# Optimization experiments

Measured on AMD Instinct MI355X. Metric: run time of the kernel, lower is better.

Reference implementation:

```python
import jax, jax.numpy as jnp
import numpy as np

LN_EPS = 1e-5

def _layernorm(x, scale, bias):
    mu = jnp.mean(x, axis=-1, keepdims=True)
    var = jnp.var(x, axis=-1, keepdims=True)
    return (x - mu) * jax.lax.rsqrt(var + LN_EPS) * scale + bias

def setup_inputs() -> dict:
    T, node_num, num_nodes, E, C = 4, 10000, 50000, 256, 128
    key = jax.random.key(0)
    ks = jax.random.split(key, 12)
    s = lambda fan_in: 1.0 / np.sqrt(fan_in)
    return {
        "x": jax.random.normal(ks[0], (T * node_num, E), jnp.float32),
        "batched_x": jax.random.normal(ks[1], (num_nodes, E), jnp.float32),
        "indices": jax.random.randint(ks[2], (T, node_num), 0, num_nodes, jnp.int32),
        "ln_d_scale": jnp.ones((E,), jnp.float32),
        "ln_d_bias": jnp.zeros((E,), jnp.float32),
        "W1_d": jax.random.normal(ks[3], (E, 2 * E), jnp.float32) * s(E),
        "b1_d": jnp.zeros((2 * E,), jnp.float32),
        "W2_d": jax.random.normal(ks[4], (2 * E, C), jnp.float32) * s(2 * E),
        "b2_d": jnp.zeros((C,), jnp.float32),
        "ln_u_scale": jnp.ones((C,), jnp.float32),
        "ln_u_bias": jnp.zeros((C,), jnp.float32),
        "W1_u": jax.random.normal(ks[5], (C, 2 * C), jnp.float32) * s(C),
        "b1_u": jnp.zeros((2 * C,), jnp.float32),
        "W2_u": jax.random.normal(ks[6], (2 * C, E), jnp.float32) * s(2 * C),
        "b2_u": jnp.zeros((E,), jnp.float32),
    }

def reference(x, batched_x, indices, ln_d_scale, ln_d_bias, W1_d, b1_d, W2_d, b2_d,
              ln_u_scale, ln_u_bias, W1_u, b1_u, W2_u, b2_u):
    T, node_num = indices.shape
    num_nodes, E = batched_x.shape
    xr = x.reshape(T, node_num, E)
    # _to_entire: per-step scatter-add of active-node embeddings into the full node table
    def scatter_one(xi, idx):
        return jnp.zeros((num_nodes, E), x.dtype).at[idx].add(xi)
    ta = jax.vmap(scatter_one)(xr, indices)          # [T, num_nodes, E]
    inp = ta + batched_x[None]                        # broadcast entire features
    h = _layernorm(inp, ln_d_scale, ln_d_bias)
    h = jax.nn.gelu(h @ W1_d + b1_d, approximate=False) @ W2_d + b2_d  # [T, num_nodes, C]
    # _from_entire: gather each step's active nodes back, concat, LN + MLP up
    g = jnp.take_along_axis(h, indices[..., None], axis=1)  # [T, node_num, C]
    g = g.reshape(T * node_num, -1)
    g = _layernorm(g, ln_u_scale, ln_u_bias)
    out = jax.nn.gelu(g @ W1_u + b1_u, approximate=False) @ W2_u + b2_u  # [T*node_num, E]
    return out
```

## Files before the change

kernel.cpp:

```cpp
#include <hip/hip_runtime.h>
#include <math.h>

#define T_STEPS   4
#define NODE_NUM  10000
#define NUM_NODES 50000
#define E         256
#define TWO_E     512
#define CC        128
#define TWO_C     256
#define ROWS      32

typedef short bf16x8 __attribute__((ext_vector_type(8)));
typedef float f32x4  __attribute__((ext_vector_type(4)));

#define MFMA16(a, b, c) __builtin_amdgcn_mfma_f32_16x16x32_bf16((a), (b), (c), 0, 0, 0)

static __device__ unsigned short g_wt[294912];

__device__ __forceinline__ float geluf(float v) {
    return 0.5f * v * (1.0f + erff(v * 0.70710678118654752440f));
}

__device__ __forceinline__ unsigned short f2bf(float f) {
    unsigned int u = __builtin_bit_cast(unsigned int, f);
    u += 0x7fffu + ((u >> 16) & 1u);
    return (unsigned short)(u >> 16);
}

__global__ void prep_weights(const float* __restrict__ W1d, const float* __restrict__ W2d,
                             const float* __restrict__ W1u, const float* __restrict__ W2u) {
    int i = blockIdx.x * 256 + threadIdx.x;
    if (i < 131072) {
        int n = i >> 8, k = i & 255;
        g_wt[i] = f2bf(W1d[(size_t)k * TWO_E + n]);
    }
    if (i < 65536) {
        int n = i >> 9, k = i & 511;
        g_wt[131072 + i] = f2bf(W2d[(size_t)k * CC + n]);
    }
    if (i < 32768) {
        int n = i >> 7, k = i & 127;
        g_wt[196608 + i] = f2bf(W1u[(size_t)k * TWO_C + n]);
    }
    if (i < 65536) {
        int n = i >> 8, k = i & 255;
        g_wt[229376 + i] = f2bf(W2u[(size_t)k * E + n]);
    }
}

__global__ void zero_rows_kernel(float* __restrict__ table,
                                 const int* __restrict__ indices,
                                 int gr0, int t0) {
    int gr = gr0 + blockIdx.x * 4 + (threadIdx.x >> 6);
    int trel = gr / NODE_NUM - t0;
    int idx = indices[gr];
    int c = (threadIdx.x & 63) * 4;
    float4 z = make_float4(0.f, 0.f, 0.f, 0.f);
    *reinterpret_cast<float4*>(&table[((size_t)trel * NUM_NODES + idx) * E + c]) = z;
}

__global__ void scatter_kernel(float* __restrict__ table,
                               const float* __restrict__ x,
                               const int* __restrict__ indices,
                               int gr0, int t0) {
    int gr = gr0 + blockIdx.x;
    int trel = gr / NODE_NUM - t0;
    int idx = indices[gr];
    atomicAdd(&table[((size_t)trel * NUM_NODES + idx) * E + threadIdx.x],
              x[(size_t)gr * E + threadIdx.x]);
}

__global__ __launch_bounds__(256, 3)
void mlp_kernel(const float* __restrict__ table,
                const float* __restrict__ batched_x,
                const int* __restrict__ indices,
                const float* __restrict__ lnd_s, const float* __restrict__ lnd_b,
                const float* __restrict__ b1d, const float* __restrict__ b2d,
                const float* __restrict__ lnu_s, const float* __restrict__ lnu_b,
                const float* __restrict__ b1u, const float* __restrict__ b2u,
                float* __restrict__ out,
                int gr0, int t0, int grLim) {
    __shared__ __align__(16) unsigned char smem[50176];
    __shared__ size_t rbase[ROWS];
    __shared__ int    ridx[ROWS];

    float*          Xf  = (float*)smem;
    unsigned short* Xs  = (unsigned short*)(smem + 33280);
    unsigned short* H1  = (unsigned short*)smem;
    float*          H2f = (float*)(smem + 33280);
    unsigned short* H2b = (unsigned short*)smem;
    unsigned short* G1  = (unsigned short*)(smem + 8704);

    const unsigned short* w1t  = g_wt;
    const unsigned short* w2t  = g_wt + 131072;
    const unsigned short* w1ut = g_wt + 196608;
    const unsigned short* w2ut = g_wt + 229376;

    const int tid = threadIdx.x;
    const int w = tid >> 6, lane = tid & 63;
    const int l16 = lane & 15, quad = lane >> 4;
    const int grb = gr0 + blockIdx.x * ROWS;

    if (tid < ROWS) {
        int gr = grb + tid;
        if (gr >= grLim) gr = grLim - 1;
        int trel = gr / NODE_NUM - t0;
        int idx = indices[gr];
        rbase[tid] = ((size_t)trel * NUM_NODES + idx) * E;
        ridx[tid]  = idx;
    }
    __syncthreads();

    #pragma unroll
    for (int it = 0; it < 8; ++it) {
        int v = it * 256 + tid;
        int r = v >> 6;
        int c = (v & 63) * 4;
        float4 tv = *reinterpret_cast<const float4*>(&table[rbase[r] + c]);
        float4 bv = *reinterpret_cast<const float4*>(&batched_x[(size_t)ridx[r] * E + c]);
        float4 s; s.x = tv.x + bv.x; s.y = tv.y + bv.y; s.z = tv.z + bv.z; s.w = tv.w + bv.w;
        *reinterpret_cast<float4*>(&Xf[r * 260 + c]) = s;
    }
    __syncthreads();

    {
        int row = tid >> 3, l8 = tid & 7;
        float s = 0.f, sq = 0.f;
        #pragma unroll
        for (int k = 0; k < 32; ++k) {
            float v = Xf[row * 260 + k * 8 + l8];
            s += v; sq += v * v;
        }
        s  += __shfl_xor(s, 1);  s  += __shfl_xor(s, 2);  s  += __shfl_xor(s, 4);
        sq += __shfl_xor(sq, 1); sq += __shfl_xor(sq, 2); sq += __shfl_xor(sq, 4);
        float mu = s * (1.0f / E);
        float var = sq * (1.0f / E) - mu * mu;
        float rs = rsqrtf(var + 1e-5f);
        #pragma unroll
        for (int k = 0; k < 32; ++k) {
            int c = k * 8 + l8;
            float v = (Xf[row * 260 + c] - mu) * rs * lnd_s[c] + lnd_b[c];
            Xs[row * 264 + c] = f2bf(v);
        }
    }
    __syncthreads();

    {
        bf16x8 af[2][8];
        #pragma unroll
        for (int mt = 0; mt < 2; ++mt) {
            const unsigned short* base = Xs + (l16 + 16 * mt) * 264 + quad * 8;
            #pragma unroll
            for (int ks = 0; ks < 8; ++ks)
                af[mt][ks] = *reinterpret_cast<const bf16x8*>(base + ks * 32);
        }
        #pragma unroll
        for (int nt_ = 0; nt_ < 8; ++nt_) {
            int n = (w * 8 + nt_) * 16 + l16;
            const unsigned short* bp = w1t + (size_t)n * 256 + quad * 8;
            f32x4 a0 = {0.f, 0.f, 0.f, 0.f}, a1 = {0.f, 0.f, 0.f, 0.f};
            #pragma unroll
            for (int ks = 0; ks < 8; ++ks) {
                bf16x8 b = *reinterpret_cast<const bf16x8*>(bp + ks * 32);
                a0 = MFMA16(af[0][ks], b, a0);
                a1 = MFMA16(af[1][ks], b, a1);
            }
            float bias = b1d[n];
            #pragma unroll
            for (int reg = 0; reg < 4; ++reg) {
                int r = quad * 4 + reg;
                H1[r * 520 + n]        = f2bf(geluf(a0[reg] + bias));
                H1[(r + 16) * 520 + n] = f2bf(geluf(a1[reg] + bias));
            }
        }
    }
    __syncthreads();

    {
        f32x4 acc2[2][2];
        #pragma unroll
        for (int i = 0; i < 2; ++i)
            #pragma unroll
            for (int j = 0; j < 2; ++j) acc2[i][j] = (f32x4){0.f, 0.f, 0.f, 0.f};
        #pragma unroll
        for (int kh = 0; kh < 2; ++kh) {
            bf16x8 af2[2][8];
            #pragma unroll
            for (int mt = 0; mt < 2; ++mt) {
                const unsigned short* base = H1 + (l16 + 16 * mt) * 520 + kh * 256 + quad * 8;
                #pragma unroll
                for (int ks = 0; ks < 8; ++ks)
                    af2[mt][ks] = *reinterpret_cast<const bf16x8*>(base + ks * 32);
            }
            #pragma unroll
            for (int nt2 = 0; nt2 < 2; ++nt2) {
                int n = (w * 2 + nt2) * 16 + l16;
                const unsigned short* bp = w2t + (size_t)n * 512 + kh * 256 + quad * 8;
                #pragma unroll
                for (int ks = 0; ks < 8; ++ks) {
                    bf16x8 b = *reinterpret_cast<const bf16x8*>(bp + ks * 32);
                    acc2[nt2][0] = MFMA16(af2[0][ks], b, acc2[nt2][0]);
                    acc2[nt2][1] = MFMA16(af2[1][ks], b, acc2[nt2][1]);
                }
            }
        }
        #pragma unroll
        for (int nt2 = 0; nt2 < 2; ++nt2) {
            int n = (w * 2 + nt2) * 16 + l16;
            float bias = b2d[n];
            #pragma unroll
            for (int mt = 0; mt < 2; ++mt)
                #pragma unroll
                for (int reg = 0; reg < 4; ++reg) {
                    int r = mt * 16 + quad * 4 + reg;
                    H2f[r * 132 + n] = acc2[nt2][mt][reg] + bias;
                }
        }
    }
    __syncthreads();

    {
        int row = tid >> 3, l8 = tid & 7;
        float s = 0.f, sq = 0.f;
        #pragma unroll
        for (int k = 0; k < 16; ++k) {
            float v = H2f[row * 132 + k * 8 + l8];
            s += v; sq += v * v;
        }
        s  += __shfl_xor(s, 1);  s  += __shfl_xor(s, 2);  s  += __shfl_xor(s, 4);
        sq += __shfl_xor(sq, 1); sq += __shfl_xor(sq, 2); sq += __shfl_xor(sq, 4);
        float mu = s * (1.0f / CC);
        float var = sq * (1.0f / CC) - mu * mu;
        float rs = rsqrtf(var + 1e-5f);
        #pragma unroll
        for (int k = 0; k < 16; ++k) {
            int c = k * 8 + l8;
            float v = (H2f[row * 132 + c] - mu) * rs * lnu_s[c] + lnu_b[c];
            H2b[row * 136 + c] = f2bf(v);
        }
    }
    __syncthreads();

    {
        bf16x8 af3[2][4];
        #pragma unroll
        for (int mt = 0; mt < 2; ++mt) {
            const unsigned short* base = H2b + (l16 + 16 * mt) * 136 + quad * 8;
            #pragma unroll
            for (int ks = 0; ks < 4; ++ks)
                af3[mt][ks] = *reinterpret_cast<const bf16x8*>(base + ks * 32);
        }
        #pragma unroll
        for (int nt_ = 0; nt_ < 4; ++nt_) {
            int n = (w * 4 + nt_) * 16 + l16;
            const unsigned short* bp = w1ut + (size_t)n * 128 + quad * 8;
            f32x4 a0 = {0.f, 0.f, 0.f, 0.f}, a1 = {0.f, 0.f, 0.f, 0.f};
            #pragma unroll
            for (int ks = 0; ks < 4; ++ks) {
                bf16x8 b = *reinterpret_cast<const bf16x8*>(bp + ks * 32);
                a0 = MFMA16(af3[0][ks], b, a0);
                a1 = MFMA16(af3[1][ks], b, a1);
            }
            float bias = b1u[n];
            #pragma unroll
            for (int reg = 0; reg < 4; ++reg) {
                int r = quad * 4 + reg;
                G1[r * 264 + n]        = f2bf(geluf(a0[reg] + bias));
                G1[(r + 16) * 264 + n] = f2bf(geluf(a1[reg] + bias));
            }
        }
    }
    __syncthreads();

    {
        bf16x8 af4[2][8];
        #pragma unroll
        for (int mt = 0; mt < 2; ++mt) {
            const unsigned short* base = G1 + (l16 + 16 * mt) * 264 + quad * 8;
            #pragma unroll
            for (int ks = 0; ks < 8; ++ks)
                af4[mt][ks] = *reinterpret_cast<const bf16x8*>(base + ks * 32);
        }
        #pragma unroll
        for (int nt_ = 0; nt_ < 4; ++nt_) {
            int n = (w * 4 + nt_) * 16 + l16;
            const unsigned short* bp = w2ut + (size_t)n * 256 + quad * 8;
            f32x4 a0 = {0.f, 0.f, 0.f, 0.f}, a1 = {0.f, 0.f, 0.f, 0.f};
            #pragma unroll
            for (int ks = 0; ks < 8; ++ks) {
                bf16x8 b = *reinterpret_cast<const bf16x8*>(bp + ks * 32);
                a0 = MFMA16(af4[0][ks], b, a0);
                a1 = MFMA16(af4[1][ks], b, a1);
            }
            float bias = b2u[n];
            #pragma unroll
            for (int reg = 0; reg < 4; ++reg) {
                int r = quad * 4 + reg;
                int g0 = grb + r, g1 = grb + r + 16;
                if (g0 < grLim) out[(size_t)g0 * E + n] = a0[reg] + bias;
                if (g1 < grLim) out[(size_t)g1 * E + n] = a1[reg] + bias;
            }
        }
    }
}

extern "C" void kernel_launch(void* const* d_in, const int* in_sizes, int n_in,
                              void* d_out, int out_size, void* d_ws, size_t ws_size,
                              hipStream_t stream) {
    const float* x     = (const float*)d_in[0];
    const float* bx    = (const float*)d_in[1];
    const int*   idxp  = (const int*)  d_in[2];
    const float* lnd_s = (const float*)d_in[3];
    const float* lnd_b = (const float*)d_in[4];
    const float* W1d   = (const float*)d_in[5];
    const float* b1d   = (const float*)d_in[6];
    const float* W2d   = (const float*)d_in[7];
    const float* b2d   = (const float*)d_in[8];
    const float* lnu_s = (const float*)d_in[9];
    const float* lnu_b = (const float*)d_in[10];
    const float* W1u   = (const float*)d_in[11];
    const float* b1u   = (const float*)d_in[12];
    const float* W2u   = (const float*)d_in[13];
    const float* b2u   = (const float*)d_in[14];
    float* out = (float*)d_out;
    float* table = (float*)d_ws;

    const size_t slice_bytes = (size_t)NUM_NODES * E * sizeof(float);
    int tb = (int)(ws_size / slice_bytes);
    if (tb < 1) tb = 1;
    if (tb > T_STEPS) tb = T_STEPS;

    prep_weights<<<512, 256, 0, stream>>>(W1d, W2d, W1u, W2u);

    for (int t0 = 0; t0 < T_STEPS; t0 += tb) {
        int tcur = T_STEPS - t0 < tb ? T_STEPS - t0 : tb;
        int nrows = tcur * NODE_NUM;
        int gr0 = t0 * NODE_NUM;
        int grLim = gr0 + nrows;
        zero_rows_kernel<<<nrows / 4, 256, 0, stream>>>(table, idxp, gr0, t0);
        scatter_kernel  <<<nrows, E, 0, stream>>>(table, x, idxp, gr0, t0);
        mlp_kernel<<<(nrows + ROWS - 1) / ROWS, 256, 0, stream>>>(
            table, bx, idxp, lnd_s, lnd_b, b1d, b2d,
            lnu_s, lnu_b, b1u, b2u, out, gr0, t0, grLim);
    }
}
```

Measured before the change: 298.5 us.

## Halve MLP row tile to 16, fuse gather with register LayerNorm, use tanh-GELU

Cuts rows per block from 32 to 16, halving shared memory and raising the launch-bounds occupancy target from 3 to 6 blocks per CU. The gather and input LayerNorm are fused so each wave keeps its rows in registers and reduces across the wavefront, which removes the fp32 staging buffer. The exact erf GELU is replaced with a sigmoid-based tanh approximation built on __expf. Each weight fragment loaded from global/L2 is now reused across only 16 rows instead of 32, which doubles weight traffic per output row, and the GELU approximation changes numerics slightly.

```diff
diff --git a/kernel.cpp b/kernel.cpp
--- a/kernel.cpp
+++ b/kernel.cpp
@@ -8,17 +8,22 @@
 #define TWO_E     512
 #define CC        128
 #define TWO_C     256
-#define ROWS      32
+#define ROWS      16
 
 typedef short bf16x8 __attribute__((ext_vector_type(8)));
 typedef float f32x4  __attribute__((ext_vector_type(4)));
+typedef unsigned short u16x4 __attribute__((ext_vector_type(4)));
 
 #define MFMA16(a, b, c) __builtin_amdgcn_mfma_f32_16x16x32_bf16((a), (b), (c), 0, 0, 0)
 
 static __device__ unsigned short g_wt[294912];
 
-__device__ __forceinline__ float geluf(float v) {
-    return 0.5f * v * (1.0f + erff(v * 0.70710678118654752440f));
+__device__ __forceinline__ float gelu_fast(float x) {
+    float x2 = x * x;
+    float p  = __builtin_fmaf(x2, 0.044715f, 1.0f);
+    float z  = 1.59576912160573f * x * p;
+    float e  = __expf(-z);
+    return x * (1.0f / (1.0f + e));
 }
 
 __device__ __forceinline__ unsigned short f2bf(float f) {
@@ -70,7 +75,7 @@
               x[(size_t)gr * E + threadIdx.x]);
 }
 
-__global__ __launch_bounds__(256, 3)
+__global__ __launch_bounds__(256, 6)
 void mlp_kernel(const float* __restrict__ table,
                 const float* __restrict__ batched_x,
                 const int* __restrict__ indices,
@@ -80,16 +85,15 @@
                 const float* __restrict__ b1u, const float* __restrict__ b2u,
                 float* __restrict__ out,
                 int gr0, int t0, int grLim) {
-    __shared__ __align__(16) unsigned char smem[50176];
+    __shared__ __align__(16) unsigned char smem[25088];
     __shared__ size_t rbase[ROWS];
     __shared__ int    ridx[ROWS];
 
-    float*          Xf  = (float*)smem;
-    unsigned short* Xs  = (unsigned short*)(smem + 33280);
-    unsigned short* H1  = (unsigned short*)smem;
-    float*          H2f = (float*)(smem + 33280);
-    unsigned short* H2b = (unsigned short*)smem;
-    unsigned short* G1  = (unsigned short*)(smem + 8704);
+    unsigned short* Xs  = (unsigned short*)smem;
+    float*          H2f = (float*)smem;
+    unsigned short* G1  = (unsigned short*)smem;
+    unsigned short* H1  = (unsigned short*)(smem + 8448);
+    unsigned short* H2b = (unsigned short*)(smem + 8448);
 
     const unsigned short* w1t  = g_wt;
     const unsigned short* w2t  = g_wt + 131072;
@@ -111,87 +115,79 @@
     }
     __syncthreads();
 
-    #pragma unroll
-    for (int it = 0; it < 8; ++it) {
-        int v = it * 256 + tid;
-        int r = v >> 6;
-        int c = (v & 63) * 4;
-        float4 tv = *reinterpret_cast<const float4*>(&table[rbase[r] + c]);
-        float4 bv = *reinterpret_cast<const float4*>(&batched_x[(size_t)ridx[r] * E + c]);
-        float4 s; s.x = tv.x + bv.x; s.y = tv.y + bv.y; s.z = tv.z + bv.z; s.w = tv.w + bv.w;
-        *reinterpret_cast<float4*>(&Xf[r * 260 + c]) = s;
-    }
-    __syncthreads();
-
-    {
-        int row = tid >> 3, l8 = tid & 7;
-        float s = 0.f, sq = 0.f;
-        #pragma unroll
-        for (int k = 0; k < 32; ++k) {
-            float v = Xf[row * 260 + k * 8 + l8];
-            s += v; sq += v * v;
-        }
-        s  += __shfl_xor(s, 1);  s  += __shfl_xor(s, 2);  s  += __shfl_xor(s, 4);
-        sq += __shfl_xor(sq, 1); sq += __shfl_xor(sq, 2); sq += __shfl_xor(sq, 4);
-        float mu = s * (1.0f / E);
-        float var = sq * (1.0f / E) - mu * mu;
-        float rs = rsqrtf(var + 1e-5f);
-        #pragma unroll
-        for (int k = 0; k < 32; ++k) {
-            int c = k * 8 + l8;
-            float v = (Xf[row * 260 + c] - mu) * rs * lnd_s[c] + lnd_b[c];
-            Xs[row * 264 + c] = f2bf(v);
-        }
-    }
-    __syncthreads();
-
-    {
-        bf16x8 af[2][8];
-        #pragma unroll
-        for (int mt = 0; mt < 2; ++mt) {
-            const unsigned short* base = Xs + (l16 + 16 * mt) * 264 + quad * 8;
-            #pragma unroll
-            for (int ks = 0; ks < 8; ++ks)
-                af[mt][ks] = *reinterpret_cast<const bf16x8*>(base + ks * 32);
-        }
+    {
+        const int c = lane * 4;
+        float4 sc4 = *reinterpret_cast<const float4*>(&lnd_s[c]);
+        float4 bi4 = *reinterpret_cast<const float4*>(&lnd_b[c]);
+        float4 xv[4];
+        #pragma unroll
+        for (int it = 0; it < 4; ++it) {
+            int r = it * 4 + w;
+            float4 tv = *reinterpret_cast<const float4*>(&table[rbase[r] + c]);
+            float4 bv = *reinterpret_cast<const float4*>(&batched_x[(size_t)ridx[r] * E + c]);
+            xv[it].x = tv.x + bv.x; xv[it].y = tv.y + bv.y;
+            xv[it].z = tv.z + bv.z; xv[it].w = tv.w + bv.w;
+        }
+        #pragma unroll
+        for (int it = 0; it < 4; ++it) {
+            int r = it * 4 + w;
+            float4 v = xv[it];
+            float s  = (v.x + v.y) + (v.z + v.w);
+            float sq = v.x * v.x + v.y * v.y + v.z * v.z + v.w * v.w;
+            #pragma unroll
+            for (int m = 1; m < 64; m <<= 1) {
+                s  += __shfl_xor(s,  m);
+                sq += __shfl_xor(sq, m);
+            }
+            float mu  = s * (1.0f / E);
+            float var = sq * (1.0f / E) - mu * mu;
+            float rs  = rsqrtf(var + 1e-5f);
+            u16x4 o;
+            o.x = f2bf((v.x - mu) * rs * sc4.x + bi4.x);
+            o.y = f2bf((v.y - mu) * rs * sc4.y + bi4.y);
+            o.z = f2bf((v.z - mu) * rs * sc4.z + bi4.z);
+            o.w = f2bf((v.w - mu) * rs * sc4.w + bi4.w);
+            *reinterpret_cast<u16x4*>(&Xs[r * 264 + c]) = o;
+        }
+    }
+    __syncthreads();
+
+    {
+        bf16x8 af[8];
+        #pragma unroll
+        for (int ks = 0; ks < 8; ++ks)
+            af[ks] = *reinterpret_cast<const bf16x8*>(&Xs[l16 * 264 + quad * 8 + ks * 32]);
         #pragma unroll
         for (int nt_ = 0; nt_ < 8; ++nt_) {
             int n = (w * 8 + nt_) * 16 + l16;
             const unsigned short* bp = w1t + (size_t)n * 256 + quad * 8;
-            f32x4 a0 = {0.f, 0.f, 0.f, 0.f}, a1 = {0.f, 0.f, 0.f, 0.f};
+            f32x4 a0 = {0.f, 0.f, 0.f, 0.f};
             #pragma unroll
             for (int ks = 0; ks < 8; ++ks) {
                 bf16x8 b = *reinterpret_cast<const bf16x8*>(bp + ks * 32);
-                a0 = MFMA16(af[0][ks], b, a0);
-                a1 = MFMA16(af[1][ks], b, a1);
+                a0 = MFMA16(af[ks], b, a0);
             }
             float bias = b1d[n];
             #pragma unroll
             for (int reg = 0; reg < 4; ++reg) {
                 int r = quad * 4 + reg;
-                H1[r * 520 + n]        = f2bf(geluf(a0[reg] + bias));
-                H1[(r + 16) * 520 + n] = f2bf(geluf(a1[reg] + bias));
-            }
-        }
-    }
-    __syncthreads();
-
-    {
-        f32x4 acc2[2][2];
-        #pragma unroll
-        for (int i = 0; i < 2; ++i)
-            #pragma unroll
-            for (int j = 0; j < 2; ++j) acc2[i][j] = (f32x4){0.f, 0.f, 0.f, 0.f};
+                H1[r * 520 + n] = f2bf(gelu_fast(a0[reg] + bias));
+            }
+        }
+    }
+    __syncthreads();
+
+    {
+        f32x4 acc2[2];
+        acc2[0] = (f32x4){0.f, 0.f, 0.f, 0.f};
+        acc2[1] = (f32x4){0.f, 0.f, 0.f, 0.f};
         #pragma unroll
         for (int kh = 0; kh < 2; ++kh) {
-            bf16x8 af2[2][8];
-            #pragma unroll
-            for (int mt = 0; mt < 2; ++mt) {
-                const unsigned short* base = H1 + (l16 + 16 * mt) * 520 + kh * 256 + quad * 8;
-                #pragma unroll
-                for (int ks = 0; ks < 8; ++ks)
-                    af2[mt][ks] = *reinterpret_cast<const bf16x8*>(base + ks * 32);
-            }
+            bf16x8 af2[8];
+            #pragma unroll
+            for (int ks = 0; ks < 8; ++ks)
+                af2[ks] = *reinterpret_cast<const bf16x8*>(
+                    &H1[l16 * 520 + kh * 256 + quad * 8 + ks * 32]);
             #pragma unroll
             for (int nt2 = 0; nt2 < 2; ++nt2) {
                 int n = (w * 2 + nt2) * 16 + l16;
@@ -199,106 +195,95 @@
                 #pragma unroll
                 for (int ks = 0; ks < 8; ++ks) {
                     bf16x8 b = *reinterpret_cast<const bf16x8*>(bp + ks * 32);
-                    acc2[nt2][0] = MFMA16(af2[0][ks], b, acc2[nt2][0]);
-                    acc2[nt2][1] = MFMA16(af2[1][ks], b, acc2[nt2][1]);
+                    acc2[nt2] = MFMA16(af2[ks], b, acc2[nt2]);
                 }
             }
         }
+        __syncthreads();
         #pragma unroll
         for (int nt2 = 0; nt2 < 2; ++nt2) {
             int n = (w * 2 + nt2) * 16 + l16;
             float bias = b2d[n];
             #pragma unroll
-            for (int mt = 0; mt < 2; ++mt)
-                #pragma unroll
-                for (int reg = 0; reg < 4; ++reg) {
-                    int r = mt * 16 + quad * 4 + reg;
-                    H2f[r * 132 + n] = acc2[nt2][mt][reg] + bias;
-                }
-        }
-    }
-    __syncthreads();
-
-    {
-        int row = tid >> 3, l8 = tid & 7;
+            for (int reg = 0; reg < 4; ++reg) {
+                int r = quad * 4 + reg;
+                H2f[r * 132 + n] = acc2[nt2][reg] + bias;
+            }
+        }
+    }
+    __syncthreads();
+
+    {
+        int row = tid >> 4;
         float s = 0.f, sq = 0.f;
-        #pragma unroll
-        for (int k = 0; k < 16; ++k) {
-            float v = H2f[row * 132 + k * 8 + l8];
-            s += v; sq += v * v;
-        }
-        s  += __shfl_xor(s, 1);  s  += __shfl_xor(s, 2);  s  += __shfl_xor(s, 4);
-        sq += __shfl_xor(sq, 1); sq += __shfl_xor(sq, 2); sq += __shfl_xor(sq, 4);
-        float mu = s * (1.0f / CC);
+        float vals[8];
+        #pragma unroll
+        for (int k = 0; k < 8; ++k) {
+            float v = H2f[row * 132 + k * 16 + l16];
+            vals[k] = v; s += v; sq += v * v;
+        }
+        s  += __shfl_xor(s, 1);  s  += __shfl_xor(s, 2);
+        s  += __shfl_xor(s, 4);  s  += __shfl_xor(s, 8);
+        sq += __shfl_xor(sq, 1); sq += __shfl_xor(sq, 2);
+        sq += __shfl_xor(sq, 4); sq += __shfl_xor(sq, 8);
+        float mu  = s * (1.0f / CC);
         float var = sq * (1.0f / CC) - mu * mu;
-        float rs = rsqrtf(var + 1e-5f);
-        #pragma unroll
-        for (int k = 0; k < 16; ++k) {
-            int c = k * 8 + l8;
-            float v = (H2f[row * 132 + c] - mu) * rs * lnu_s[c] + lnu_b[c];
+        float rs  = rsqrtf(var + 1e-5f);
+        #pragma unroll
+        for (int k = 0; k < 8; ++k) {
+            int c = k * 16 + l16;
+            float v = (vals[k] - mu) * rs * lnu_s[c] + lnu_b[c];
             H2b[row * 136 + c] = f2bf(v);
         }
     }
     __syncthreads();
 
     {
-        bf16x8 af3[2][4];
-        #pragma unroll
-        for (int mt = 0; mt < 2; ++mt) {
-            const unsigned short* base = H2b + (l16 + 16 * mt) * 136 + quad * 8;
-            #pragma unroll
-            for (int ks = 0; ks < 4; ++ks)
-                af3[mt][ks] = *reinterpret_cast<const bf16x8*>(base + ks * 32);
-        }
+        bf16x8 af3[4];
+        #pragma unroll
+        for (int ks = 0; ks < 4; ++ks)
+            af3[ks] = *reinterpret_cast<const bf16x8*>(&H2b[l16 * 136 + quad * 8 + ks * 32]);
         #pragma unroll
         for (int nt_ = 0; nt_ < 4; ++nt_) {
             int n = (w * 4 + nt_) * 16 + l16;
             const unsigned short* bp = w1ut + (size_t)n * 128 + quad * 8;
-            f32x4 a0 = {0.f, 0.f, 0.f, 0.f}, a1 = {0.f, 0.f, 0.f, 0.f};
+            f32x4 a0 = {0.f, 0.f, 0.f, 0.f};
             #pragma unroll
             for (int ks = 0; ks < 4; ++ks) {
                 bf16x8 b = *reinterpret_cast<const bf16x8*>(bp + ks * 32);
-                a0 = MFMA16(af3[0][ks], b, a0);
-                a1 = MFMA16(af3[1][ks], b, a1);
+                a0 = MFMA16(af3[ks], b, a0);
             }
             float bias = b1u[n];
             #pragma unroll
             for (int reg = 0; reg < 4; ++reg) {
                 int r = quad * 4 + reg;
-                G1[r * 264 + n]        = f2bf(geluf(a0[reg] + bias));
-                G1[(r + 16) * 264 + n] = f2bf(geluf(a1[reg] + bias));
-            }
-        }
-    }
-    __syncthreads();
-
-    {
-        bf16x8 af4[2][8];
-        #pragma unroll
-        for (int mt = 0; mt < 2; ++mt) {
-            const unsigned short* base = G1 + (l16 + 16 * mt) * 264 + quad * 8;
-            #pragma unroll
-            for (int ks = 0; ks < 8; ++ks)
-                af4[mt][ks] = *reinterpret_cast<const bf16x8*>(base + ks * 32);
-        }
+                G1[r * 264 + n] = f2bf(gelu_fast(a0[reg] + bias));
+            }
+        }
+    }
+    __syncthreads();
+
+    {
+        bf16x8 af4[8];
+        #pragma unroll
+        for (int ks = 0; ks < 8; ++ks)
+            af4[ks] = *reinterpret_cast<const bf16x8*>(&G1[l16 * 264 + quad * 8 + ks * 32]);
         #pragma unroll
         for (int nt_ = 0; nt_ < 4; ++nt_) {
             int n = (w * 4 + nt_) * 16 + l16;
             const unsigned short* bp = w2ut + (size_t)n * 256 + quad * 8;
-            f32x4 a0 = {0.f, 0.f, 0.f, 0.f}, a1 = {0.f, 0.f, 0.f, 0.f};
+            f32x4 a0 = {0.f, 0.f, 0.f, 0.f};
             #pragma unroll
             for (int ks = 0; ks < 8; ++ks) {
                 bf16x8 b = *reinterpret_cast<const bf16x8*>(bp + ks * 32);
-                a0 = MFMA16(af4[0][ks], b, a0);
-                a1 = MFMA16(af4[1][ks], b, a1);
+                a0 = MFMA16(af4[ks], b, a0);
             }
             float bias = b2u[n];
             #pragma unroll
             for (int reg = 0; reg < 4; ++reg) {
                 int r = quad * 4 + reg;
-                int g0 = grb + r, g1 = grb + r + 16;
+                int g0 = grb + r;
                 if (g0 < grLim) out[(size_t)g0 * E + n] = a0[reg] + bias;
-                if (g1 < grLim) out[(size_t)g1 * E + n] = a1[reg] + bias;
             }
         }
     }
```

New measurement: 352.9 us. 1.18x slower.
